# Performance work log

Measured on AMD Instinct MI355X. Metric: run time of the kernel, lower is better.

Reference implementation:

```python
import jax, jax.numpy as jnp
import numpy as np

INITRANGE = 0.04
STEPS = 8
# arch[2i] = predecessor state index (0..i), arch[2i+1] = activation id
ARCH = [0, 0, 0, 1, 1, 2, 1, 3, 2, 0, 2, 1, 3, 2, 4, 3]
ACTS = [jnp.tanh, jax.nn.relu, jax.nn.sigmoid, lambda x: x]

T, B, NINP, NHID = 512, 64, 512, 512


def setup_inputs() -> dict:
    key = jax.random.key(0)
    k0, k1, k2, k3 = jax.random.split(key, 4)
    inputs = jax.random.normal(k0, (T, B, NINP), jnp.float32)
    hidden = jax.random.normal(k1, (1, B, NHID), jnp.float32)
    W0 = jax.random.uniform(k2, (NINP + NHID, 2 * NHID), jnp.float32, -INITRANGE, INITRANGE)
    Ws = jax.random.uniform(k3, (STEPS, NHID, 2 * NHID), jnp.float32, -INITRANGE, INITRANGE)
    return {"inputs": inputs, "hidden": hidden, "W0": W0, "Ws": Ws}


def _cell(x, h_prev, W0, Ws):
    nhid = h_prev.shape[-1]
    # init state: gated convex combination of h_prev and candidate
    xh = jnp.concatenate([x, h_prev], axis=-1)          # [B, ninp+nhid]
    ch0 = xh @ W0                                       # [B, 2*nhid]
    c0 = jax.nn.sigmoid(ch0[:, :nhid])
    h0 = jnp.tanh(ch0[:, nhid:])
    s0 = h_prev + c0 * (h0 - h_prev)
    states = [s0]
    for i in range(STEPS):
        pred, act = ARCH[2 * i], ARCH[2 * i + 1]
        s_prev = states[pred]
        ch = s_prev @ Ws[i]                             # [B, 2*nhid]
        c = jax.nn.sigmoid(ch[:, :nhid])
        h = ACTS[act](ch[:, nhid:])
        states.append(s_prev + c * (h - s_prev))
    # mean over the STEPS intermediate states (excluding s0)
    return jnp.mean(jnp.stack(states[1:], axis=-1), axis=-1)


def reference(inputs, hidden, W0, Ws):
    # inputs: [T,B,ninp]; hidden: [1,B,nhid] (eval mode: no dropout masks)
    def step(h, x):
        h_new = _cell(x, h, W0, Ws)
        return h_new, h_new

    _, hiddens = jax.lax.scan(step, hidden[0], inputs)  # [T,B,nhid]
    return hiddens, hiddens[-1][None]
```

## Files before the change

kernel.cpp:

```cpp
#include <hip/hip_runtime.h>

typedef unsigned short u16;
typedef unsigned int   u32;
typedef unsigned long long u64;

typedef __attribute__((ext_vector_type(8))) _Float16 half8;
typedef __attribute__((ext_vector_type(4))) float    f32x4;

#define T_STEPS 512

__device__ __forceinline__ f32x4 mfma16(uint4 a, uint4 b, f32x4 c) {
  union { uint4 u; half8 h; } A, B;
  A.u = a; B.u = b;
  return __builtin_amdgcn_mfma_f32_16x16x32_f16(A.h, B.h, c, 0, 0, 0);
}
__device__ __forceinline__ u16 f2h(float f) {
  union { _Float16 h; u16 u; } x; x.h = (_Float16)f; return x.u;
}
__device__ __forceinline__ float h2f(u16 v) {
  union { _Float16 h; u16 u; } x; x.u = v; return (float)x.h;
}
__device__ __forceinline__ void sth(u16* p, u16 v) {
  __hip_atomic_store(p, v, __ATOMIC_RELAXED, __HIP_MEMORY_SCOPE_AGENT);
}
__device__ __forceinline__ u64 ld8(const u64* p) {
  return __hip_atomic_load(p, __ATOMIC_RELAXED, __HIP_MEMORY_SCOPE_AGENT);
}
__device__ __forceinline__ float sigm(float x)  { return 1.0f / (1.0f + __expf(-x)); }
__device__ __forceinline__ float tanhx(float x) { return 2.0f / (1.0f + __expf(-2.0f * x)) - 1.0f; }

__device__ __forceinline__ void frag_load(uint4* af, const u16* buf, int rowoff) {
#pragma unroll
  for (int kc = 0; kc < 16; ++kc) {
    const u64* p = (const u64*)(buf + rowoff + kc * 32);
    u64 lo = ld8(p), hi = ld8(p + 1);
    af[kc].x = (u32)lo; af[kc].y = (u32)(lo >> 32);
    af[kc].z = (u32)hi; af[kc].w = (u32)(hi >> 32);
  }
}
__device__ __forceinline__ f32x4 mm(const uint4* af, const uint4* lw, int slice, int lane) {
  f32x4 acc = {0.f, 0.f, 0.f, 0.f};
#pragma unroll
  for (int kc = 0; kc < 16; ++kc)
    acc = mfma16(af[kc], lw[slice * 1024 + kc * 64 + lane], acc);
  return acc;
}

__device__ __forceinline__ void wave_signal(u32* slot, u32 epoch) {
  asm volatile("s_waitcnt vmcnt(0) lgkmcnt(0)" ::: "memory");
  if ((threadIdx.x & 63) == 0)
    __hip_atomic_store(slot, epoch, __ATOMIC_RELAXED, __HIP_MEMORY_SCOPE_AGENT);
}
__device__ __forceinline__ void wave_wait(const u32* base, u32 epoch) {
  const u32* p = base + (size_t)(threadIdx.x & 63) * 16;
  while (__hip_atomic_load(p, __ATOMIC_RELAXED, __HIP_MEMORY_SCOPE_AGENT) < epoch) {}
  asm volatile("" ::: "memory");
}

__global__ __launch_bounds__(256) void pack_kernel(const float* __restrict__ w0,
                                                   const float* __restrict__ wsrc,
                                                   u16* __restrict__ wp) {
  int gid = blockIdx.x * 256 + threadIdx.x;
  int w = gid >> 16, c = gid & 65535;
  int jb = c >> 10, kc = (c >> 6) & 15, lane = c & 63;
  int nl = lane & 15, kh = lane >> 4;
  int n = (nl < 8) ? (jb * 8 + nl) : (512 + jb * 8 + nl - 8);
  int k = kc * 32 + kh * 8;
  const float* s;
  if (w == 0)      s = w0 + (size_t)k * 1024 + n;
  else if (w == 1) s = w0 + (size_t)(512 + k) * 1024 + n;
  else             s = wsrc + (size_t)(w - 2) * 524288 + (size_t)k * 1024 + n;
  u32 e[8];
#pragma unroll
  for (int i = 0; i < 8; ++i) e[i] = (u32)f2h(s[(size_t)i * 1024]);
  uint4 v;
  v.x = e[0] | (e[1] << 16); v.y = e[2] | (e[3] << 16);
  v.z = e[4] | (e[5] << 16); v.w = e[6] | (e[7] << 16);
  ((uint4*)wp)[gid] = v;
}

__global__ __launch_bounds__(256) void xw_kernel(const float* __restrict__ x,
                                                 const u16* __restrict__ wp,
                                                 u64* __restrict__ xwp) {
  __shared__ uint4 smem[4096];
  int t = blockIdx.x >> 4, jbg = blockIdx.x & 15;
  int tid = threadIdx.x, lane = tid & 63, wv = tid >> 6;
  const float* src = x + (size_t)t * 64 * 512;
#pragma unroll
  for (int it = 0; it < 16; ++it) {
    int d = tid + it * 256;
    int ln = d & 63, kcL = (d >> 6) & 15, mtL = d >> 10;
    int lm = mtL * 16 + (ln & 15);
    int k8 = kcL * 4 + (ln >> 4);
    const float* p = src + (size_t)lm * 512 + (size_t)k8 * 8;
    float4 a = *(const float4*)p;
    float4 b = *(const float4*)(p + 4);
    uint4 v;
    v.x = (u32)f2h(a.x) | ((u32)f2h(a.y) << 16);
    v.y = (u32)f2h(a.z) | ((u32)f2h(a.w) << 16);
    v.z = (u32)f2h(b.x) | ((u32)f2h(b.y) << 16);
    v.w = (u32)f2h(b.z) | ((u32)f2h(b.w) << 16);
    smem[d] = v;
  }
  __syncthreads();
  int jb = jbg * 4 + wv;
  const uint4* bp = (const uint4*)wp + (size_t)jb * 1024;
  f32x4 acc[4] = {{0,0,0,0},{0,0,0,0},{0,0,0,0},{0,0,0,0}};
#pragma unroll
  for (int kc = 0; kc < 16; ++kc) {
    uint4 b = bp[kc * 64 + lane];
#pragma unroll
    for (int m4 = 0; m4 < 4; ++m4)
      acc[m4] = mfma16(smem[(m4 * 16 + kc) * 64 + lane], b, acc[m4]);
  }
#pragma unroll
  for (int m4 = 0; m4 < 4; ++m4) {
    u32 lo = (u32)f2h(acc[m4][0]) | ((u32)f2h(acc[m4][1]) << 16);
    u32 hi = (u32)f2h(acc[m4][2]) | ((u32)f2h(acc[m4][3]) << 16);
    xwp[((size_t)(t * 64 + jb) * 4 + m4) * 64 + lane] = (u64)lo | ((u64)hi << 32);
  }
}

__global__ __launch_bounds__(256) void init_hh(const float* __restrict__ h, u16* __restrict__ hh) {
  int i = blockIdx.x * 256 + threadIdx.x;
  if (i < 32768) hh[i] = f2h(h[i]);
}

__global__ __launch_bounds__(256) void recur_kernel(
    const u64* __restrict__ xwp, const float* __restrict__ h_in,
    const u16* __restrict__ wp,
    u16* __restrict__ sh,
    u16* __restrict__ hh,
    u32* __restrict__ bar,
    float* __restrict__ out) {
  extern __shared__ char smem_raw[];
  uint4* lw     = (uint4*)smem_raw;
  float* scr_s0 = (float*)(smem_raw + 147456);
  float* scr_s4 = (float*)(smem_raw + 148480);
  float* scr_m1 = (float*)(smem_raw + 149504);
  u32*   lflag  = (u32*)(smem_raw + 150528);

  const int wg = blockIdx.x;
  const int jb = wg & 63, g = wg >> 6;
  const int rb = g * 32;
  const int tid = threadIdx.x;
  const int lane = tid & 63;
  const int wid = tid >> 6;
  const int mt = wid & 1, sel = wid >> 1;
  const int n = lane & 15, r0 = (lane >> 4) * 4;
  const int rowoff = (rb + mt * 16 + n) * 512 + (lane >> 4) * 8;
  const int jj = jb * 8 + (n & 7);
  const int sbase = (mt * 16 + r0) * 8 + (n & 7);
  u32* flg = bar + (size_t)g * 10240;
  const uint4* wp4 = (const uint4*)wp;
  u32* chA = flg + (0 + mt) * 1024;
  u32* chB = flg + (2 + 2 * sel + mt) * 1024;
  u32* chC = flg + (6 + mt) * 1024;
  u32* chD = flg + (8 + mt) * 1024;

  for (int idx = tid; idx < 9216; idx += 256) {
    int s = idx >> 10, rem = idx & 1023;
    lw[idx] = wp4[(size_t)(1 + s) * 65536 + (size_t)jb * 1024 + rem];
  }
  if (tid < 2) lflag[tid] = 0;
  __syncthreads();

  float h_reg[4];
  float mean[4] = {0, 0, 0, 0};
  float s0r[4], s1r[4], s3r[4];
  u64 xv = 0;
  if (sel == 0)
    xv = xwp[((size_t)(0 * 64 + jb) * 4 + (g * 2 + mt)) * 64 + lane];

  for (int t = 0; t < T_STEPS; ++t) {
    const u32 ep = (u32)t + 1;
    uint4 af[16];
    if (sel == 0) {
      wave_wait(chD, (u32)t);
      frag_load(af, hh, rowoff);
      f32x4 acc = mm(af, lw, 0, lane);
      float v[4], part[4];
#pragma unroll
      for (int i = 0; i < 4; ++i) v[i] = acc[i] + h2f((u16)(xv >> (16 * i)));
#pragma unroll
      for (int i = 0; i < 4; ++i) part[i] = __shfl_xor(v[i], 8);
      if (n < 8) {
#pragma unroll
        for (int i = 0; i < 4; ++i) {
          int m = rb + mt * 16 + r0 + i;
          float hp = (t == 0) ? h_in[m * 512 + jj] : h_reg[i];
          float s0 = hp + sigm(v[i]) * (tanhx(part[i]) - hp);
          s0r[i] = s0;
          scr_s0[sbase + i * 8] = s0;
          sth(sh + m * 512 + jj, f2h(s0));
        }
      }
      wave_signal(chA + jb * 16, ep);
      int tn = (t < T_STEPS - 1) ? t + 1 : t;
      xv = xwp[((size_t)(tn * 64 + jb) * 4 + (g * 2 + mt)) * 64 + lane];
    }
    wave_wait(chA, ep);
    frag_load(af, sh, rowoff);
    {
      f32x4 acc = mm(af, lw, 1 + sel, lane);
      float part[4];
#pragma unroll
      for (int i = 0; i < 4; ++i) part[i] = __shfl_xor(acc[i], 8);
      if (n < 8) {
#pragma unroll
        for (int i = 0; i < 4; ++i) {
          int m = rb + mt * 16 + r0 + i;
          float sp = (sel == 0) ? s0r[i] : scr_s0[sbase + i * 8];
          float hc = (sel == 0) ? tanhx(part[i]) : fmaxf(part[i], 0.f);
          float sn = sp + sigm(acc[i]) * (hc - sp);
          s1r[i] = sn;
          mean[i] = sn;
          sth(sh + (size_t)(1 + sel) * 32768 + m * 512 + jj, f2h(sn));
        }
      }
    }
    wave_signal(chB + jb * 16, ep);
    wave_wait(chB, ep);
    frag_load(af, sh + (size_t)(1 + sel) * 32768, rowoff);
    {
      f32x4 a0 = {0, 0, 0, 0}, a1 = {0, 0, 0, 0};
#pragma unroll
      for (int kc = 0; kc < 16; ++kc) {
        uint4 a = af[kc];
        a0 = mfma16(a, lw[(3 + 2 * sel) * 1024 + kc * 64 + lane], a0);
        a1 = mfma16(a, lw[(4 + 2 * sel) * 1024 + kc * 64 + lane], a1);
      }
      float p0[4], p1[4];
#pragma unroll
      for (int i = 0; i < 4; ++i) { p0[i] = __shfl_xor(a0[i], 8); p1[i] = __shfl_xor(a1[i], 8); }
      if (n < 8) {
#pragma unroll
        for (int i = 0; i < 4; ++i) {
          int m = rb + mt * 16 + r0 + i;
          float sp = s1r[i];
          if (sel == 0) {
            float s3 = sp + sigm(a0[i]) * (sigm(p0[i]) - sp);
            float s4 = sp + sigm(a1[i]) * (p1[i] - sp);
            mean[i] += s3 + s4;
            s3r[i] = s3;
            scr_s4[sbase + i * 8] = s4;
            sth(sh + (size_t)3 * 32768 + m * 512 + jj, f2h(s3));
            sth(sh + (size_t)4 * 32768 + m * 512 + jj, f2h(s4));
          } else {
            float s5 = sp + sigm(a0[i]) * (tanhx(p0[i]) - sp);
            float s6 = sp + sigm(a1[i]) * (fmaxf(p1[i], 0.f) - sp);
            mean[i] += s5 + s6;
          }
        }
      }
    }
    if (sel == 0) wave_signal(chC + jb * 16, ep);
    wave_wait(chC, ep);
    frag_load(af, sh + (size_t)(3 + sel) * 32768, rowoff);
    {
      f32x4 acc = mm(af, lw, 7 + sel, lane);
      float part[4];
#pragma unroll
      for (int i = 0; i < 4; ++i) part[i] = __shfl_xor(acc[i], 8);
      if (sel == 1) {
        if (n < 8) {
#pragma unroll
          for (int i = 0; i < 4; ++i) {
            float sp = scr_s4[sbase + i * 8];
            float s8 = sp + sigm(acc[i]) * (part[i] - sp);
            scr_m1[sbase + i * 8] = mean[i] + s8;
          }
        }
        asm volatile("s_waitcnt lgkmcnt(0)" ::: "memory");
        if (lane == 0)
          __hip_atomic_store(&lflag[mt], ep, __ATOMIC_RELAXED, __HIP_MEMORY_SCOPE_WORKGROUP);
      } else {
        while (__hip_atomic_load(&lflag[mt], __ATOMIC_RELAXED,
                                 __HIP_MEMORY_SCOPE_WORKGROUP) < ep) {}
        asm volatile("" ::: "memory");
        if (n < 8) {
#pragma unroll
          for (int i = 0; i < 4; ++i) {
            int m = rb + mt * 16 + r0 + i;
            float s7 = s3r[i] + sigm(acc[i]) * (sigm(part[i]) - s3r[i]);
            float hn = (mean[i] + s7 + scr_m1[sbase + i * 8]) * 0.125f;
            h_reg[i] = hn;
            sth(hh + m * 512 + jj, f2h(hn));
            out[((size_t)t * 64 + m) * 512 + jj] = hn;
            if (t == T_STEPS - 1) out[(size_t)T_STEPS * 64 * 512 + m * 512 + jj] = hn;
          }
        }
        wave_signal(chD + jb * 16, ep);
      }
    }
  }
}

extern "C" void kernel_launch(void* const* d_in, const int* in_sizes, int n_in,
                              void* d_out, int out_size, void* d_ws, size_t ws_size,
                              hipStream_t stream) {
  const float* x_in = (const float*)d_in[0];
  const float* h_in = (const float*)d_in[1];
  const float* w0   = (const float*)d_in[2];
  const float* wsrc = (const float*)d_in[3];
  float* out = (float*)d_out;
  char* ws = (char*)d_ws;

  const size_t O_BAR = 0;
  const size_t O_WP  = 98304;
  const size_t O_XWP = O_WP + 10485760;
  const size_t O_SH  = O_XWP + 67108864;
  const size_t O_HH  = O_SH + 327680;
  const size_t NEED  = O_HH + 65536;
  if (ws_size < NEED) return;

  u32* bar = (u32*)(ws + O_BAR);
  u16* wp  = (u16*)(ws + O_WP);
  u64* xwp = (u64*)(ws + O_XWP);
  u16* sh  = (u16*)(ws + O_SH);
  u16* hh  = (u16*)(ws + O_HH);

  const int LDS_BYTES = 151552;
  hipFuncSetAttribute((const void*)recur_kernel,
                      hipFuncAttributeMaxDynamicSharedMemorySize, LDS_BYTES);

  hipMemsetAsync(bar, 0, 98304, stream);
  pack_kernel<<<dim3(2560), dim3(256), 0, stream>>>(w0, wsrc, wp);
  xw_kernel<<<dim3(8192), dim3(256), 0, stream>>>(x_in, wp, xwp);
  init_hh<<<dim3(128), dim3(256), 0, stream>>>(h_in, hh);
  recur_kernel<<<dim3(128), dim3(256), LDS_BYTES, stream>>>(xwp, h_in, wp, sh, hh, bar, out);
}
```

Before: 11.85 ms.

## Replace flag barriers with epoch-tagged data packets polled directly

```diff
diff --git a/kernel.cpp b/kernel.cpp
--- a/kernel.cpp
+++ b/kernel.cpp
@@ -6,11 +6,12 @@
 
 typedef __attribute__((ext_vector_type(8))) _Float16 half8;
 typedef __attribute__((ext_vector_type(4))) float    f32x4;
+typedef __attribute__((ext_vector_type(4))) u32      u32x4;
 
 #define T_STEPS 512
 
-__device__ __forceinline__ f32x4 mfma16(uint4 a, uint4 b, f32x4 c) {
-  union { uint4 u; half8 h; } A, B;
+__device__ __forceinline__ f32x4 mfma16(u32x4 a, u32x4 b, f32x4 c) {
+  union { u32x4 u; half8 h; } A, B;
   A.u = a; B.u = b;
   return __builtin_amdgcn_mfma_f32_16x16x32_f16(A.h, B.h, c, 0, 0, 0);
 }
@@ -20,25 +21,10 @@
 __device__ __forceinline__ float h2f(u16 v) {
   union { _Float16 h; u16 u; } x; x.u = v; return (float)x.h;
 }
-__device__ __forceinline__ void sth(u16* p, u16 v) {
-  __hip_atomic_store(p, v, __ATOMIC_RELAXED, __HIP_MEMORY_SCOPE_AGENT);
-}
-__device__ __forceinline__ u64 ld8(const u64* p) {
-  return __hip_atomic_load(p, __ATOMIC_RELAXED, __HIP_MEMORY_SCOPE_AGENT);
-}
 __device__ __forceinline__ float sigm(float x)  { return 1.0f / (1.0f + __expf(-x)); }
 __device__ __forceinline__ float tanhx(float x) { return 2.0f / (1.0f + __expf(-2.0f * x)) - 1.0f; }
 
-__device__ __forceinline__ void frag_load(uint4* af, const u16* buf, int rowoff) {
-#pragma unroll
-  for (int kc = 0; kc < 16; ++kc) {
-    const u64* p = (const u64*)(buf + rowoff + kc * 32);
-    u64 lo = ld8(p), hi = ld8(p + 1);
-    af[kc].x = (u32)lo; af[kc].y = (u32)(lo >> 32);
-    af[kc].z = (u32)hi; af[kc].w = (u32)(hi >> 32);
-  }
-}
-__device__ __forceinline__ f32x4 mm(const uint4* af, const uint4* lw, int slice, int lane) {
+__device__ __forceinline__ f32x4 mm(const u32x4* af, const u32x4* lw, int slice, int lane) {
   f32x4 acc = {0.f, 0.f, 0.f, 0.f};
 #pragma unroll
   for (int kc = 0; kc < 16; ++kc)
@@ -46,15 +32,62 @@
   return acc;
 }
 
-__device__ __forceinline__ void wave_signal(u32* slot, u32 epoch) {
-  asm volatile("s_waitcnt vmcnt(0) lgkmcnt(0)" ::: "memory");
-  if ((threadIdx.x & 63) == 0)
-    __hip_atomic_store(slot, epoch, __ATOMIC_RELAXED, __HIP_MEMORY_SCOPE_AGENT);
-}
-__device__ __forceinline__ void wave_wait(const u32* base, u32 epoch) {
-  const u32* p = base + (size_t)(threadIdx.x & 63) * 16;
-  while (__hip_atomic_load(p, __ATOMIC_RELAXED, __HIP_MEMORY_SCOPE_AGENT) < epoch) {}
-  asm volatile("" ::: "memory");
+
+#define PK_FOREACH(F) \
+  F(0, "0", "16")        F(1, "128", "144")     F(2, "256", "272")     F(3, "384", "400")     \
+  F(4, "512", "528")     F(5, "640", "656")     F(6, "768", "784")     F(7, "896", "912")     \
+  F(8, "1024", "1040")   F(9, "1152", "1168")   F(10, "1280", "1296")  F(11, "1408", "1424")  \
+  F(12, "1536", "1552")  F(13, "1664", "1680")  F(14, "1792", "1808")  F(15, "1920", "1936")
+
+__device__ __forceinline__ void poll_frags(u32x4* af, const u32x4* bp, u32 want) {
+  u32x4 t0[16], t1[16];
+#define PK_LD(k, O0, O1) \
+  asm volatile("global_load_dwordx4 %0, %1, off offset:" O0 " sc0 sc1" \
+               : "=v"(t0[k]) : "v"(bp) : "memory"); \
+  asm volatile("global_load_dwordx4 %0, %1, off offset:" O1 " sc0 sc1" \
+               : "=v"(t1[k]) : "v"(bp) : "memory");
+#define PK_LAU(k, O0, O1) asm volatile("" : "+v"(t0[k]), "+v"(t1[k]));
+#define PK_CHK(k, O0, O1) \
+  if (__any((int)((t0[k].z < want) || (t1[k].z < want)))) { PK_LD(k, O0, O1) nd = 1; }
+  PK_FOREACH(PK_LD)
+  asm volatile("s_waitcnt vmcnt(0)" ::: "memory");
+  PK_FOREACH(PK_LAU)
+  for (;;) {
+    int nd = 0;
+    PK_FOREACH(PK_CHK)
+    if (!nd) break;
+    asm volatile("s_waitcnt vmcnt(0)" ::: "memory");
+    PK_FOREACH(PK_LAU)
+  }
+#pragma unroll
+  for (int k = 0; k < 16; ++k) {
+    af[k].x = t0[k].x; af[k].y = t0[k].y;
+    af[k].z = t1[k].x; af[k].w = t1[k].y;
+  }
+#undef PK_LD
+#undef PK_LAU
+#undef PK_CHK
+}
+
+__device__ __forceinline__ void pkt_emit(u32x4* sbase, u16* scrw, int lane, int mrow0,
+                                         int jb, u32 ep, const float* v) {
+  const int n = lane & 15;
+  const int r0 = (lane >> 4) * 4;
+  if (n < 8) {
+#pragma unroll
+    for (int i = 0; i < 4; ++i) scrw[(r0 + i) * 8 + n] = f2h(v[i]);
+  }
+  asm volatile("s_waitcnt lgkmcnt(0)" ::: "memory");
+  __builtin_amdgcn_sched_barrier(0);
+  if (n < 8) {
+    const int q = (lane >> 4) * 8 + n;
+    const int r = q >> 1, hh = q & 1;
+    const u32* d = (const u32*)(scrw + r * 8 + hh * 4);
+    u32x4 pk;
+    pk.x = d[0]; pk.y = d[1]; pk.z = ep; pk.w = 0u;
+    u32x4* addr = sbase + ((mrow0 + r) * 128 + jb * 2 + hh);
+    asm volatile("global_store_dwordx4 %0, %1, off sc0 sc1" :: "v"(addr), "v"(pk) : "memory");
+  }
 }
 
 __global__ __launch_bounds__(256) void pack_kernel(const float* __restrict__ w0,
@@ -109,9 +142,12 @@
 #pragma unroll
   for (int kc = 0; kc < 16; ++kc) {
     uint4 b = bp[kc * 64 + lane];
-#pragma unroll
-    for (int m4 = 0; m4 < 4; ++m4)
-      acc[m4] = mfma16(smem[(m4 * 16 + kc) * 64 + lane], b, acc[m4]);
+    union { uint4 u; half8 h; } B; B.u = b;
+#pragma unroll
+    for (int m4 = 0; m4 < 4; ++m4) {
+      union { uint4 u; half8 h; } A; A.u = smem[(m4 * 16 + kc) * 64 + lane];
+      acc[m4] = __builtin_amdgcn_mfma_f32_16x16x32_f16(A.h, B.h, acc[m4], 0, 0, 0);
+    }
   }
 #pragma unroll
   for (int m4 = 0; m4 < 4; ++m4) {
@@ -121,42 +157,44 @@
   }
 }
 
-__global__ __launch_bounds__(256) void init_hh(const float* __restrict__ h, u16* __restrict__ hh) {
+__global__ __launch_bounds__(256) void init_hp(const float* __restrict__ h,
+                                               u32x4* __restrict__ pkt) {
   int i = blockIdx.x * 256 + threadIdx.x;
-  if (i < 32768) hh[i] = f2h(h[i]);
-}
-
-__global__ __launch_bounds__(256) void recur_kernel(
+  int m = i >> 7, rest = i & 127;
+  int col = (rest >> 1) * 8 + (rest & 1) * 4;
+  const float* s = h + (size_t)m * 512 + col;
+  u32x4 pk;
+  pk.x = (u32)f2h(s[0]) | ((u32)f2h(s[1]) << 16);
+  pk.y = (u32)f2h(s[2]) | ((u32)f2h(s[3]) << 16);
+  pk.z = 0u; pk.w = 0u;
+  pkt[(size_t)5 * 8192 + i] = pk;
+}
+
+__global__ __launch_bounds__(256, 1) void recur_kernel(
     const u64* __restrict__ xwp, const float* __restrict__ h_in,
-    const u16* __restrict__ wp,
-    u16* __restrict__ sh,
-    u16* __restrict__ hh,
-    u32* __restrict__ bar,
+    const u16* __restrict__ wp, u32x4* __restrict__ pkt,
     float* __restrict__ out) {
   extern __shared__ char smem_raw[];
-  uint4* lw     = (uint4*)smem_raw;
+  u32x4* lw     = (u32x4*)smem_raw;
   float* scr_s0 = (float*)(smem_raw + 147456);
   float* scr_s4 = (float*)(smem_raw + 148480);
   float* scr_m1 = (float*)(smem_raw + 149504);
-  u32*   lflag  = (u32*)(smem_raw + 150528);
+  u16*   scrw   = (u16*)(smem_raw + 150528);
+  u32*   lflag  = (u32*)(smem_raw + 151552);
 
   const int wg = blockIdx.x;
   const int jb = wg & 63, g = wg >> 6;
-  const int rb = g * 32;
   const int tid = threadIdx.x;
   const int lane = tid & 63;
   const int wid = tid >> 6;
   const int mt = wid & 1, sel = wid >> 1;
   const int n = lane & 15, r0 = (lane >> 4) * 4;
-  const int rowoff = (rb + mt * 16 + n) * 512 + (lane >> 4) * 8;
+  const int mrow0 = g * 32 + mt * 16;
+  const int mbase = (mrow0 + n) * 128 + (lane >> 4) * 2;
   const int jj = jb * 8 + (n & 7);
   const int sbase = (mt * 16 + r0) * 8 + (n & 7);
-  u32* flg = bar + (size_t)g * 10240;
-  const uint4* wp4 = (const uint4*)wp;
-  u32* chA = flg + (0 + mt) * 1024;
-  u32* chB = flg + (2 + 2 * sel + mt) * 1024;
-  u32* chC = flg + (6 + mt) * 1024;
-  u32* chD = flg + (8 + mt) * 1024;
+  u16* myscrw = scrw + wid * 128;
+  const u32x4* wp4 = (const u32x4*)wp;
 
   for (int idx = tid; idx < 9216; idx += 256) {
     int s = idx >> 10, rem = idx & 1023;
@@ -172,14 +210,13 @@
   if (sel == 0)
     xv = xwp[((size_t)(0 * 64 + jb) * 4 + (g * 2 + mt)) * 64 + lane];
 
+  u32x4 af[16];
   for (int t = 0; t < T_STEPS; ++t) {
     const u32 ep = (u32)t + 1;
-    uint4 af[16];
     if (sel == 0) {
-      wave_wait(chD, (u32)t);
-      frag_load(af, hh, rowoff);
+      poll_frags(af, pkt + (size_t)5 * 8192 + mbase, (u32)t);
       f32x4 acc = mm(af, lw, 0, lane);
-      float v[4], part[4];
+      float v[4], part[4], s0v[4];
 #pragma unroll
       for (int i = 0; i < 4; ++i) v[i] = acc[i] + h2f((u16)(xv >> (16 * i)));
 #pragma unroll
@@ -187,66 +224,66 @@
       if (n < 8) {
 #pragma unroll
         for (int i = 0; i < 4; ++i) {
-          int m = rb + mt * 16 + r0 + i;
-          float hp = (t == 0) ? h_in[m * 512 + jj] : h_reg[i];
+          float hp = (t == 0) ? h_in[(size_t)(mrow0 + r0 + i) * 512 + jj] : h_reg[i];
           float s0 = hp + sigm(v[i]) * (tanhx(part[i]) - hp);
-          s0r[i] = s0;
+          s0v[i] = s0; s0r[i] = s0;
           scr_s0[sbase + i * 8] = s0;
-          sth(sh + m * 512 + jj, f2h(s0));
-        }
-      }
-      wave_signal(chA + jb * 16, ep);
+        }
+      }
+      pkt_emit(pkt, myscrw, lane, mrow0, jb, ep, s0v);
       int tn = (t < T_STEPS - 1) ? t + 1 : t;
       xv = xwp[((size_t)(tn * 64 + jb) * 4 + (g * 2 + mt)) * 64 + lane];
     }
-    wave_wait(chA, ep);
-    frag_load(af, sh, rowoff);
+    poll_frags(af, pkt + mbase, ep);
     {
       f32x4 acc = mm(af, lw, 1 + sel, lane);
-      float part[4];
+      float part[4], sv[4];
 #pragma unroll
       for (int i = 0; i < 4; ++i) part[i] = __shfl_xor(acc[i], 8);
       if (n < 8) {
 #pragma unroll
         for (int i = 0; i < 4; ++i) {
-          int m = rb + mt * 16 + r0 + i;
           float sp = (sel == 0) ? s0r[i] : scr_s0[sbase + i * 8];
           float hc = (sel == 0) ? tanhx(part[i]) : fmaxf(part[i], 0.f);
           float sn = sp + sigm(acc[i]) * (hc - sp);
-          s1r[i] = sn;
-          mean[i] = sn;
-          sth(sh + (size_t)(1 + sel) * 32768 + m * 512 + jj, f2h(sn));
-        }
-      }
-    }
-    wave_signal(chB + jb * 16, ep);
-    wave_wait(chB, ep);
-    frag_load(af, sh + (size_t)(1 + sel) * 32768, rowoff);
+          s1r[i] = sn; mean[i] = sn; sv[i] = sn;
+        }
+      }
+      pkt_emit(pkt + (size_t)(1 + sel) * 8192, myscrw, lane, mrow0, jb, ep, sv);
+    }
+    poll_frags(af, pkt + (size_t)(1 + sel) * 8192 + mbase, ep);
     {
       f32x4 a0 = {0, 0, 0, 0}, a1 = {0, 0, 0, 0};
 #pragma unroll
       for (int kc = 0; kc < 16; ++kc) {
-        uint4 a = af[kc];
+        u32x4 a = af[kc];
         a0 = mfma16(a, lw[(3 + 2 * sel) * 1024 + kc * 64 + lane], a0);
         a1 = mfma16(a, lw[(4 + 2 * sel) * 1024 + kc * 64 + lane], a1);
       }
       float p0[4], p1[4];
 #pragma unroll
       for (int i = 0; i < 4; ++i) { p0[i] = __shfl_xor(a0[i], 8); p1[i] = __shfl_xor(a1[i], 8); }
-      if (n < 8) {
-#pragma unroll
-        for (int i = 0; i < 4; ++i) {
-          int m = rb + mt * 16 + r0 + i;
-          float sp = s1r[i];
-          if (sel == 0) {
+      if (sel == 0) {
+        float s3v[4], s4v[4];
+        if (n < 8) {
+#pragma unroll
+          for (int i = 0; i < 4; ++i) {
+            float sp = s1r[i];
             float s3 = sp + sigm(a0[i]) * (sigm(p0[i]) - sp);
             float s4 = sp + sigm(a1[i]) * (p1[i] - sp);
             mean[i] += s3 + s4;
             s3r[i] = s3;
+            s3v[i] = s3; s4v[i] = s4;
             scr_s4[sbase + i * 8] = s4;
-            sth(sh + (size_t)3 * 32768 + m * 512 + jj, f2h(s3));
-            sth(sh + (size_t)4 * 32768 + m * 512 + jj, f2h(s4));
-          } else {
+          }
+        }
+        pkt_emit(pkt + (size_t)3 * 8192, myscrw, lane, mrow0, jb, ep, s3v);
+        pkt_emit(pkt + (size_t)4 * 8192, myscrw, lane, mrow0, jb, ep, s4v);
+      } else {
+        if (n < 8) {
+#pragma unroll
+          for (int i = 0; i < 4; ++i) {
+            float sp = s1r[i];
             float s5 = sp + sigm(a0[i]) * (tanhx(p0[i]) - sp);
             float s6 = sp + sigm(a1[i]) * (fmaxf(p1[i], 0.f) - sp);
             mean[i] += s5 + s6;
@@ -254,9 +291,7 @@
         }
       }
     }
-    if (sel == 0) wave_signal(chC + jb * 16, ep);
-    wave_wait(chC, ep);
-    frag_load(af, sh + (size_t)(3 + sel) * 32768, rowoff);
+    poll_frags(af, pkt + (size_t)(3 + sel) * 8192 + mbase, ep);
     {
       f32x4 acc = mm(af, lw, 7 + sel, lane);
       float part[4];
@@ -278,19 +313,19 @@
         while (__hip_atomic_load(&lflag[mt], __ATOMIC_RELAXED,
                                  __HIP_MEMORY_SCOPE_WORKGROUP) < ep) {}
         asm volatile("" ::: "memory");
+        float hv[4];
         if (n < 8) {
 #pragma unroll
           for (int i = 0; i < 4; ++i) {
-            int m = rb + mt * 16 + r0 + i;
+            int m = mrow0 + r0 + i;
             float s7 = s3r[i] + sigm(acc[i]) * (sigm(part[i]) - s3r[i]);
             float hn = (mean[i] + s7 + scr_m1[sbase + i * 8]) * 0.125f;
-            h_reg[i] = hn;
-            sth(hh + m * 512 + jj, f2h(hn));
+            h_reg[i] = hn; hv[i] = hn;
             out[((size_t)t * 64 + m) * 512 + jj] = hn;
-            if (t == T_STEPS - 1) out[(size_t)T_STEPS * 64 * 512 + m * 512 + jj] = hn;
+            if (t == T_STEPS - 1) out[(size_t)T_STEPS * 64 * 512 + (size_t)m * 512 + jj] = hn;
           }
         }
-        wave_signal(chD + jb * 16, ep);
+        pkt_emit(pkt + (size_t)5 * 8192, myscrw, lane, mrow0, jb, ep, hv);
       }
     }
   }
@@ -306,27 +341,22 @@
   float* out = (float*)d_out;
   char* ws = (char*)d_ws;
 
-  const size_t O_BAR = 0;
-  const size_t O_WP  = 98304;
-  const size_t O_XWP = O_WP + 10485760;
-  const size_t O_SH  = O_XWP + 67108864;
-  const size_t O_HH  = O_SH + 327680;
-  const size_t NEED  = O_HH + 65536;
+  const size_t O_WP  = 0;
+  const size_t O_XWP = 10485760;
+  const size_t NEED  = O_XWP + 67108864;
   if (ws_size < NEED) return;
 
-  u32* bar = (u32*)(ws + O_BAR);
-  u16* wp  = (u16*)(ws + O_WP);
-  u64* xwp = (u64*)(ws + O_XWP);
-  u16* sh  = (u16*)(ws + O_SH);
-  u16* hh  = (u16*)(ws + O_HH);
-
-  const int LDS_BYTES = 151552;
+  u16*   wp  = (u16*)(ws + O_WP);
+  u32x4* pkt = (u32x4*)(ws + O_WP);
+  u64*   xwp = (u64*)(ws + O_XWP);
+
+  const int LDS_BYTES = 151568;
   hipFuncSetAttribute((const void*)recur_kernel,
                       hipFuncAttributeMaxDynamicSharedMemorySize, LDS_BYTES);
 
-  hipMemsetAsync(bar, 0, 98304, stream);
   pack_kernel<<<dim3(2560), dim3(256), 0, stream>>>(w0, wsrc, wp);
   xw_kernel<<<dim3(8192), dim3(256), 0, stream>>>(x_in, wp, xwp);
-  init_hh<<<dim3(128), dim3(256), 0, stream>>>(h_in, hh);
-  recur_kernel<<<dim3(128), dim3(256), LDS_BYTES, stream>>>(xwp, h_in, wp, sh, hh, bar, out);
-}
+  hipMemsetAsync(pkt, 0, 786432, stream);
+  init_hp<<<dim3(32), dim3(256), 0, stream>>>(h_in, pkt);
+  recur_kernel<<<dim3(128), dim3(256), LDS_BYTES, stream>>>(xwp, h_in, wp, pkt, out);
+}
```

Measured after the change: 17.56 ms. 1.48x slower.
